# Performance work log

Hardware: AMD Instinct MI355X
Metric: run time of the kernel (lower is better)

## Reference

```python
import jax, jax.numpy as jnp
import numpy as np

EMBED_DIM = 1024
NUM_HEADS = 16
HEAD_DIM = EMBED_DIM // NUM_HEADS
D_FF = 4096
N, T, S = 4, 2048, 2048


def _linear_params(key, d_in, d_out):
    k1, k2 = jax.random.split(key)
    bound = 1.0 / np.sqrt(d_in)
    W = jax.random.uniform(k1, (d_in, d_out), minval=-bound, maxval=bound, dtype=jnp.float32)
    b = jax.random.uniform(k2, (d_out,), minval=-bound, maxval=bound, dtype=jnp.float32)
    return W, b


def setup_inputs() -> dict:
    key = jax.random.key(0)
    ks = jax.random.split(key, 20)
    inp = {
        'tgt': jax.random.normal(ks[0], (N, T, EMBED_DIM), dtype=jnp.float32),
        'memory': jax.random.normal(ks[1], (N, S, EMBED_DIM), dtype=jnp.float32),
        'tgt_mask': jnp.tril(jnp.ones((T, T), dtype=jnp.float32)),
    }
    # self-attn params
    for i, nm in enumerate(['sa_Wq', 'sa_Wk', 'sa_Wv', 'sa_A', 'ca_Wq', 'ca_Wk', 'ca_Wv', 'ca_A']):
        W, b = _linear_params(ks[2 + i], EMBED_DIM, EMBED_DIM)
        inp[nm] = W
        inp[nm + '_b'] = b
    W1, b1 = _linear_params(ks[10], EMBED_DIM, D_FF)
    W2, b2 = _linear_params(ks[11], D_FF, EMBED_DIM)
    inp.update(lin1_W=W1, lin1_b=b1, lin2_W=W2, lin2_b=b2)
    for i in (1, 2, 3):
        inp[f'ln{i}_g'] = jnp.ones((EMBED_DIM,), dtype=jnp.float32)
        inp[f'ln{i}_b'] = jnp.zeros((EMBED_DIM,), dtype=jnp.float32)
    return inp


def _layer_norm(x, g, b, eps=1e-5):
    mu = jnp.mean(x, axis=-1, keepdims=True)
    var = jnp.var(x, axis=-1, keepdims=True)
    return (x - mu) * jax.lax.rsqrt(var + eps) * g + b


def _mha(query, key, value, Wq, bq, Wk, bk, Wv, bv, Wa, ba, mask=None):
    Nq, Tq, D = query.shape
    Tk = key.shape[1]
    q = (query @ Wq + bq).reshape(Nq, Tq, NUM_HEADS, HEAD_DIM)
    k = (key @ Wk + bk).reshape(Nq, Tk, NUM_HEADS, HEAD_DIM)
    v = (value @ Wv + bv).reshape(Nq, Tk, NUM_HEADS, HEAD_DIM)
    attn = jnp.einsum('bthd,bshd->bhts', q, k) / np.sqrt(HEAD_DIM)
    if mask is not None:
        attn = jnp.where(mask == 0, -jnp.inf, attn)
    score = jax.nn.softmax(attn, axis=-1)
    y = jnp.einsum('bhts,bshd->bthd', score, v).reshape(Nq, Tq, D)
    return y @ Wa + ba


def reference(tgt, memory, tgt_mask,
              sa_Wq, sa_Wq_b, sa_Wk, sa_Wk_b, sa_Wv, sa_Wv_b, sa_A, sa_A_b,
              ca_Wq, ca_Wq_b, ca_Wk, ca_Wk_b, ca_Wv, ca_Wv_b, ca_A, ca_A_b,
              lin1_W, lin1_b, lin2_W, lin2_b,
              ln1_g, ln1_b, ln2_g, ln2_b, ln3_g, ln3_b):
    t2 = _mha(tgt, tgt, tgt, sa_Wq, sa_Wq_b, sa_Wk, sa_Wk_b, sa_Wv, sa_Wv_b, sa_A, sa_A_b, tgt_mask)
    x = _layer_norm(tgt + t2, ln1_g, ln1_b)
    t2 = _mha(x, memory, memory, ca_Wq, ca_Wq_b, ca_Wk, ca_Wk_b, ca_Wv, ca_Wv_b, ca_A, ca_A_b)
    x = _layer_norm(x + t2, ln2_g, ln2_b)
    t2 = jax.nn.relu(x @ lin1_W + lin1_b) @ lin2_W + lin2_b
    return _layer_norm(x + t2, ln3_g, ln3_b)
```

## Files before the change

kernel.cpp:

```cpp
#include <hip/hip_runtime.h>

typedef __bf16 bf16;
typedef __bf16 bf16x4 __attribute__((ext_vector_type(4)));
typedef __bf16 bf16x8 __attribute__((ext_vector_type(8)));
typedef float  f32x4  __attribute__((ext_vector_type(4)));

#define EMBED 1024
#define HEADS 16
#define HDIM  64
#define DFF   4096
#define BATCH 4
#define SEQ   2048
#define MROWS 8192

__global__ __launch_bounds__(256) void cvt_kernel(
    const float* __restrict__ x, bf16* __restrict__ y, int n)
{
  int i = (blockIdx.x * 256 + threadIdx.x) * 8;
  if (i >= n) return;
  float4 a = *(const float4*)(x + i);
  float4 b = *(const float4*)(x + i + 4);
  bf16x8 v;
  v[0] = (bf16)a.x; v[1] = (bf16)a.y; v[2] = (bf16)a.z; v[3] = (bf16)a.w;
  v[4] = (bf16)b.x; v[5] = (bf16)b.y; v[6] = (bf16)b.z; v[7] = (bf16)b.w;
  *(bf16x8*)(y + i) = v;
}

__global__ __launch_bounds__(256) void wt_kernel(
    const float* __restrict__ W, bf16* __restrict__ Wt, int K, int N)
{
  __shared__ __align__(16) float Ls[64 * 68];
  const int k0 = blockIdx.x * 64, n0 = blockIdx.y * 64;
  const int ty = threadIdx.x >> 4, tx = threadIdx.x & 15;
  #pragma unroll
  for (int r = 0; r < 4; ++r) {
    const int k = ty + r * 16;
    float4 v = *(const float4*)(W + (size_t)(k0 + k) * N + n0 + tx * 4);
    *(float4*)(Ls + k * 68 + tx * 4) = v;
  }
  __syncthreads();
  #pragma unroll
  for (int it = 0; it < 2; ++it) {
    const int c = it * 256 + threadIdx.x;
    const int n = c >> 3, kc = (c & 7) * 8;
    bf16x8 v;
    #pragma unroll
    for (int j = 0; j < 8; ++j) v[j] = (bf16)Ls[(kc + j) * 68 + n];
    *(bf16x8*)(Wt + (size_t)(n0 + n) * K + k0 + kc) = v;
  }
}

__global__ void cat3_kernel(float* __restrict__ dst, const float* __restrict__ a,
                            const float* __restrict__ b, const float* __restrict__ c, int n)
{
  int i = blockIdx.x * 256 + threadIdx.x;
  if (i < n) dst[i] = a[i];
  else if (i < 2 * n) dst[i] = b[i - n];
  else if (c && i < 3 * n) dst[i] = c[i - 2 * n];
}

__global__ __launch_bounds__(256) void vtr_kernel(
    const bf16* __restrict__ V, int ldv, bf16* __restrict__ Vt, int Skv)
{
  __shared__ __align__(16) bf16 Ls[64 * 72];
  const int k0 = blockIdx.x * 64;
  const int bh = blockIdx.y, b = bh >> 4, h = bh & 15;
  const int t = threadIdx.x;
  {
    const int key = t >> 2, dc = (t & 3) * 16;
    const bf16* src = V + (size_t)(b * Skv + k0 + key) * ldv + h * HDIM + dc;
    bf16x8 a0 = *(const bf16x8*)src;
    bf16x8 a1 = *(const bf16x8*)(src + 8);
    *(bf16x8*)(Ls + key * 72 + dc) = a0;
    *(bf16x8*)(Ls + key * 72 + dc + 8) = a1;
  }
  __syncthreads();
  {
    const int d = t >> 2, kc = (t & 3) * 16;
    bf16x8 v0, v1;
    #pragma unroll
    for (int j = 0; j < 8; ++j) v0[j] = Ls[(kc + j) * 72 + d];
    #pragma unroll
    for (int j = 0; j < 8; ++j) v1[j] = Ls[(kc + 8 + j) * 72 + d];
    bf16* dst = Vt + ((size_t)(bh * HDIM + d)) * Skv + k0 + kc;
    *(bf16x8*)dst = v0;
    *(bf16x8*)(dst + 8) = v1;
  }
}

__device__ __forceinline__ void gll16(const bf16* g, bf16* l) {
  __builtin_amdgcn_global_load_lds(
      (const __attribute__((address_space(1))) unsigned*)g,
      (__attribute__((address_space(3))) unsigned*)l, 16, 0, 0);
}

__global__ __launch_bounds__(256) void gemm128(
    const bf16* __restrict__ A, int lda, const bf16* __restrict__ Bt, int ldb,
    const float* __restrict__ bias, const bf16* __restrict__ res_b,
    const float* __restrict__ res_f, bf16* __restrict__ out_b,
    float* __restrict__ out_f, int N, int K, int relu)
{
  __shared__ __align__(16) bf16 As[128 * 32];
  __shared__ __align__(16) bf16 Bs[128 * 32];
  const int tid  = threadIdx.x;
  const int lane = tid & 63, wave = tid >> 6;
  const int quad = lane >> 4, l16 = lane & 15;
  const int wm = wave & 1, wn = wave >> 1;
  const int m0 = blockIdx.y * 128, n0 = blockIdx.x * 128;

  const int c0row = tid >> 2, c0kc = (tid & 3) * 8;
  const int c1row = (256 + tid) >> 2, c1kc = c0kc;

  f32x4 acc[4][4];
  #pragma unroll
  for (int i = 0; i < 4; ++i)
    #pragma unroll
    for (int j = 0; j < 4; ++j) acc[i][j] = f32x4{0, 0, 0, 0};

  for (int k0 = 0; k0 < K; k0 += 32) {
    gll16(A  + (size_t)(m0 + c0row) * lda + k0 + c0kc, As + (size_t)(wave * 64) * 8);
    gll16(Bt + (size_t)(n0 + c0row) * ldb + k0 + c0kc, Bs + (size_t)(wave * 64) * 8);
    gll16(A  + (size_t)(m0 + c1row) * lda + k0 + c1kc, As + (size_t)(256 + wave * 64) * 8);
    gll16(Bt + (size_t)(n0 + c1row) * ldb + k0 + c1kc, Bs + (size_t)(256 + wave * 64) * 8);
    __syncthreads();

    bf16x8 af[4], bfr[4];
    #pragma unroll
    for (int i = 0; i < 4; ++i)
      af[i] = *(const bf16x8*)(As + (wm * 64 + i * 16 + l16) * 32 + quad * 8);
    #pragma unroll
    for (int j = 0; j < 4; ++j)
      bfr[j] = *(const bf16x8*)(Bs + (wn * 64 + j * 16 + l16) * 32 + quad * 8);
    #pragma unroll
    for (int i = 0; i < 4; ++i)
      #pragma unroll
      for (int j = 0; j < 4; ++j)
        acc[i][j] = __builtin_amdgcn_mfma_f32_16x16x32_bf16(af[i], bfr[j], acc[i][j], 0, 0, 0);
    __syncthreads();
  }

  #pragma unroll
  for (int j = 0; j < 4; ++j) {
    const int col = n0 + wn * 64 + j * 16 + l16;
    const float bv = bias ? bias[col] : 0.f;
    #pragma unroll
    for (int i = 0; i < 4; ++i) {
      #pragma unroll
      for (int r = 0; r < 4; ++r) {
        const int row = m0 + wm * 64 + i * 16 + quad * 4 + r;
        const size_t idx = (size_t)row * N + col;
        float v = acc[i][j][r] + bv;
        if (res_b) v += (float)res_b[idx];
        if (res_f) v += res_f[idx];
        if (relu)  v = fmaxf(v, 0.f);
        if (out_b) out_b[idx] = (bf16)v;
        if (out_f) out_f[idx] = v;
      }
    }
  }
}

__global__ __launch_bounds__(256) void ln_kernel(
    const float* __restrict__ x, const float* __restrict__ g, const float* __restrict__ b,
    bf16* __restrict__ out_b, float* __restrict__ out_f)
{
  __shared__ float red[8];
  const int tid = threadIdx.x, lane = tid & 63, wave = tid >> 6;
  const float* xr = x + (size_t)blockIdx.x * EMBED;
  float4 v = *(const float4*)(xr + tid * 4);
  float vv[4] = {v.x, v.y, v.z, v.w};
  float s  = vv[0] + vv[1] + vv[2] + vv[3];
  float s2 = vv[0]*vv[0] + vv[1]*vv[1] + vv[2]*vv[2] + vv[3]*vv[3];
  #pragma unroll
  for (int off = 32; off >= 1; off >>= 1) {
    s  += __shfl_xor(s, off);
    s2 += __shfl_xor(s2, off);
  }
  if (lane == 0) { red[wave] = s; red[4 + wave] = s2; }
  __syncthreads();
  s  = red[0] + red[1] + red[2] + red[3];
  s2 = red[4] + red[5] + red[6] + red[7];
  const float mu  = s * (1.f / EMBED);
  const float var = s2 * (1.f / EMBED) - mu * mu;
  const float rs  = rsqrtf(fmaxf(var, 0.f) + 1e-5f);
  #pragma unroll
  for (int i = 0; i < 4; ++i) {
    const int col = tid * 4 + i;
    const float o = (vv[i] - mu) * rs * g[col] + b[col];
    const size_t idx = (size_t)blockIdx.x * EMBED + col;
    if (out_b) out_b[idx] = (bf16)o;
    if (out_f) out_f[idx] = o;
  }
}

__global__ __launch_bounds__(256) void fattn_kernel(
    const bf16* __restrict__ Q, int ldq, const bf16* __restrict__ K, int ldk,
    const bf16* __restrict__ Vt, bf16* __restrict__ Y, int Skv, int causal)
{
  constexpr int PLD = 72;
  __shared__ __align__(16) bf16 Ks[2][64 * 64];
  __shared__ __align__(16) bf16 Vs[2][64 * 64];
  __shared__ __align__(16) bf16 Ps[4 * 32 * PLD];

  const int tid  = threadIdx.x;
  const int lane = tid & 63, wave = tid >> 6;
  const int quad = lane >> 4, l16 = lane & 15;
  const int q0 = blockIdx.x * 128;
  const int bh = blockIdx.y, b = bh >> 4, h = bh & 15;
  const int wq0 = q0 + wave * 32;

  const bf16* Kb = K + (size_t)b * Skv * ldk + h * HDIM;
  const bf16* Vb = Vt + (size_t)(bh * HDIM) * Skv;

  const int sr = lane >> 3;
  const int se = ((lane & 7) ^ sr) << 3;

  const int sw  = l16 & 7;
  const int co0 = (quad ^ sw) << 3;
  const int co1 = ((4 + quad) ^ sw) << 3;

  auto stage = [&](int kt, int buf) {
    const int k0 = kt * 64;
    const int r0 = wave * 16;
    gll16(Kb + (size_t)(k0 + r0 + sr) * ldk + se,     &Ks[buf][(r0)     * 64]);
    gll16(Kb + (size_t)(k0 + r0 + 8 + sr) * ldk + se, &Ks[buf][(r0 + 8) * 64]);
    gll16(Vb + (size_t)(r0 + sr) * Skv + k0 + se,     &Vs[buf][(r0)     * 64]);
    gll16(Vb + (size_t)(r0 + 8 + sr) * Skv + k0 + se, &Vs[buf][(r0 + 8) * 64]);
  };

  bf16x8 qf[2][2];
  #pragma unroll
  for (int i = 0; i < 2; ++i) {
    const bf16* qp = Q + (size_t)(b * SEQ + wq0 + i * 16 + l16) * ldq + h * HDIM;
    qf[i][0] = *(const bf16x8*)(qp + quad * 8);
    qf[i][1] = *(const bf16x8*)(qp + 32 + quad * 8);
  }

  f32x4 O[2][4];
  float m_run[2], l_run[2];
  #pragma unroll
  for (int i = 0; i < 2; ++i)
    #pragma unroll
    for (int nt = 0; nt < 4; ++nt) O[i][nt] = f32x4{0, 0, 0, 0};
  #pragma unroll
  for (int i = 0; i < 2; ++i) { m_run[i] = -1e30f; l_run[i] = 0.f; }

  bf16* Pw = Ps + wave * 32 * PLD;
  const int nkt = causal ? (q0 / 64 + 2) : (Skv / 64);

  stage(0, 0);
  __syncthreads();

  for (int kt = 0; kt < nkt; ++kt) {
    const int cur = kt & 1;
    const int k0 = kt * 64;
    if (kt + 1 < nkt) stage(kt + 1, cur ^ 1);

    const bf16* Kc = Ks[cur];
    const bf16* Vc = Vs[cur];

    f32x4 s[2][4];
    __builtin_amdgcn_s_setprio(1);
    #pragma unroll
    for (int nt = 0; nt < 4; ++nt) {
      const int row = nt * 16 + l16;
      bf16x8 kf0 = *(const bf16x8*)(Kc + row * 64 + co0);
      bf16x8 kf1 = *(const bf16x8*)(Kc + row * 64 + co1);
      #pragma unroll
      for (int i = 0; i < 2; ++i) {
        f32x4 t = f32x4{0, 0, 0, 0};
        t = __builtin_amdgcn_mfma_f32_16x16x32_bf16(kf0, qf[i][0], t, 0, 0, 0);
        t = __builtin_amdgcn_mfma_f32_16x16x32_bf16(kf1, qf[i][1], t, 0, 0, 0);
        s[i][nt] = t;
      }
    }
    __builtin_amdgcn_s_setprio(0);

    const bool diag = causal && (k0 + 63 > wq0);
    #pragma unroll
    for (int i = 0; i < 2; ++i) {
      const int q = wq0 + i * 16 + l16;
      #pragma unroll
      for (int nt = 0; nt < 4; ++nt) {
        #pragma unroll
        for (int r = 0; r < 4; ++r) {
          float v = s[i][nt][r] * 0.125f;
          const int key = k0 + nt * 16 + quad * 4 + r;
          if (diag && key > q) v = -1e30f;
          s[i][nt][r] = v;
        }
      }
    }

    #pragma unroll
    for (int i = 0; i < 2; ++i) {
      float pm = s[i][0][0];
      #pragma unroll
      for (int nt = 0; nt < 4; ++nt)
        #pragma unroll
        for (int r = 0; r < 4; ++r) pm = fmaxf(pm, s[i][nt][r]);
      pm = fmaxf(pm, __shfl_xor(pm, 16));
      pm = fmaxf(pm, __shfl_xor(pm, 32));
      const float m_new = fmaxf(m_run[i], pm);
      const float al = __expf(m_run[i] - m_new);
      m_run[i] = m_new;
      float ls = 0.f;
      #pragma unroll
      for (int nt = 0; nt < 4; ++nt) {
        #pragma unroll
        for (int r = 0; r < 4; ++r) {
          const float e = __expf(s[i][nt][r] - m_new);
          s[i][nt][r] = e;
          ls += e;
        }
      }
      ls += __shfl_xor(ls, 16);
      ls += __shfl_xor(ls, 32);
      l_run[i] = l_run[i] * al + ls;
      #pragma unroll
      for (int nt = 0; nt < 4; ++nt) {
        bf16x4 pk;
        pk[0] = (bf16)s[i][nt][0]; pk[1] = (bf16)s[i][nt][1];
        pk[2] = (bf16)s[i][nt][2]; pk[3] = (bf16)s[i][nt][3];
        *(bf16x4*)(Pw + (i * 16 + l16) * PLD + nt * 16 + quad * 4) = pk;
      }
      float alo[4];
      #pragma unroll
      for (int r = 0; r < 4; ++r) alo[r] = __shfl(al, quad * 4 + r);
      #pragma unroll
      for (int nt = 0; nt < 4; ++nt)
        #pragma unroll
        for (int r = 0; r < 4; ++r) O[i][nt][r] *= alo[r];
    }

    bf16x8 pf[2][2];
    #pragma unroll
    for (int i = 0; i < 2; ++i) {
      pf[i][0] = *(const bf16x8*)(Pw + (i * 16 + l16) * PLD + quad * 8);
      pf[i][1] = *(const bf16x8*)(Pw + (i * 16 + l16) * PLD + 32 + quad * 8);
    }
    __builtin_amdgcn_s_setprio(1);
    #pragma unroll
    for (int nt = 0; nt < 4; ++nt) {
      const int row = nt * 16 + l16;
      bf16x8 vf0 = *(const bf16x8*)(Vc + row * 64 + co0);
      bf16x8 vf1 = *(const bf16x8*)(Vc + row * 64 + co1);
      #pragma unroll
      for (int i = 0; i < 2; ++i) {
        O[i][nt] = __builtin_amdgcn_mfma_f32_16x16x32_bf16(pf[i][0], vf0, O[i][nt], 0, 0, 0);
        O[i][nt] = __builtin_amdgcn_mfma_f32_16x16x32_bf16(pf[i][1], vf1, O[i][nt], 0, 0, 0);
      }
    }
    __builtin_amdgcn_s_setprio(0);
    __syncthreads();
  }

  #pragma unroll
  for (int i = 0; i < 2; ++i) {
    float inv[4];
    #pragma unroll
    for (int r = 0; r < 4; ++r) {
      const float lv = __shfl(l_run[i], quad * 4 + r);
      inv[r] = 1.f / lv;
    }
    #pragma unroll
    for (int nt = 0; nt < 4; ++nt) {
      #pragma unroll
      for (int r = 0; r < 4; ++r) {
        const int q = wq0 + i * 16 + quad * 4 + r;
        Y[((size_t)(b * SEQ + q)) * EMBED + h * HDIM + nt * 16 + l16] = (bf16)(O[i][nt][r] * inv[r]);
      }
    }
  }
}

__global__ void fill_kernel(float* out, float v, int n) {
  int i = blockIdx.x * 256 + threadIdx.x;
  if (i < n) out[i] = v;
}

extern "C" void kernel_launch(void* const* d_in, const int* in_sizes, int n_in,
                              void* d_out, int out_size, void* d_ws, size_t ws_size,
                              hipStream_t stream)
{
  const float* tgt    = (const float*)d_in[0];
  const float* mem    = (const float*)d_in[1];
  const float* sa_Wq  = (const float*)d_in[3];
  const float* sa_Wqb = (const float*)d_in[4];
  const float* sa_Wk  = (const float*)d_in[5];
  const float* sa_Wkb = (const float*)d_in[6];
  const float* sa_Wv  = (const float*)d_in[7];
  const float* sa_Wvb = (const float*)d_in[8];
  const float* sa_A   = (const float*)d_in[9];
  const float* sa_Ab  = (const float*)d_in[10];
  const float* ca_Wq  = (const float*)d_in[11];
  const float* ca_Wqb = (const float*)d_in[12];
  const float* ca_Wk  = (const float*)d_in[13];
  const float* ca_Wkb = (const float*)d_in[14];
  const float* ca_Wv  = (const float*)d_in[15];
  const float* ca_Wvb = (const float*)d_in[16];
  const float* ca_A   = (const float*)d_in[17];
  const float* ca_Ab  = (const float*)d_in[18];
  const float* l1W    = (const float*)d_in[19];
  const float* l1b    = (const float*)d_in[20];
  const float* l2W    = (const float*)d_in[21];
  const float* l2b    = (const float*)d_in[22];
  const float* g1     = (const float*)d_in[23];
  const float* b1     = (const float*)d_in[24];
  const float* g2     = (const float*)d_in[25];
  const float* b2     = (const float*)d_in[26];
  const float* g3     = (const float*)d_in[27];
  const float* b3     = (const float*)d_in[28];

  const size_t MB = 1024 * 1024;
  const size_t NEED = 80 * MB + 4096;
  if (ws_size < NEED) {
    fill_kernel<<<(out_size + 255) / 256, 256, 0, stream>>>((float*)d_out, 3.0f, out_size);
    return;
  }

  char* ws = (char*)d_ws;
  const size_t MD = (size_t)MROWS * EMBED;
  bf16*  qkv   = (bf16*)ws;
  bf16*  yb    = (bf16*)(ws + 48 * MB);
  bf16*  wqkvt = (bf16*)(ws + 48 * MB);
  float* qkvbias = (float*)(ws + 54 * MB + 512 * 1024);
  bf16*  kvb   = (bf16*)ws;
  bf16*  qB    = (bf16*)(ws + 32 * MB);
  bf16*  wkvt  = (bf16*)(ws + 48 * MB);
  bf16*  wqt   = (bf16*)(ws + 52 * MB);
  float* kvbias = (float*)(ws + 54 * MB + 512 * 1024);
  bf16*  awt   = (bf16*)ws;
  bf16*  xb    = (bf16*)(ws + 64 * MB);
  bf16*  hb    = (bf16*)ws;
  bf16*  l1t   = (bf16*)(ws + 32 * MB);
  bf16*  l2t   = (bf16*)(ws + 40 * MB);
  float* P   = (float*)d_out;
  bf16*  inb = (bf16*)d_out;
  bf16*  vtg = (bf16*)((char*)d_out + 16 * MB);

  dim3 blk(256);
  dim3 gQKV(3072 / 128, MROWS / 128);
  dim3 gKV(2048 / 128, MROWS / 128);
  dim3 gEE(EMBED / 128, MROWS / 128);
  dim3 gF1(2048 / 128, MROWS / 128);
  dim3 gAT(SEQ / 128, BATCH * HEADS);
  dim3 gVT(SEQ / 64, BATCH * HEADS);
  dim3 gWee(16, 16);
  const int ncv = (int)(MD / 8 / 256);

  cvt_kernel<<<ncv, blk, 0, stream>>>(tgt, inb, (int)MD);
  wt_kernel<<<gWee, blk, 0, stream>>>(sa_Wq, wqkvt, EMBED, EMBED);
  wt_kernel<<<gWee, blk, 0, stream>>>(sa_Wk, wqkvt + 1024 * 1024, EMBED, EMBED);
  wt_kernel<<<gWee, blk, 0, stream>>>(sa_Wv, wqkvt + 2 * 1024 * 1024, EMBED, EMBED);
  cat3_kernel<<<12, blk, 0, stream>>>(qkvbias, sa_Wqb, sa_Wkb, sa_Wvb, EMBED);
  gemm128<<<gQKV, blk, 0, stream>>>(inb, EMBED, wqkvt, EMBED, qkvbias, nullptr, nullptr, qkv, nullptr, 3072, EMBED, 0);
  vtr_kernel<<<gVT, blk, 0, stream>>>(qkv + 2048, 3072, vtg, SEQ);
  fattn_kernel<<<gAT, blk, 0, stream>>>(qkv, 3072, qkv + 1024, 3072, vtg, yb, SEQ, 1);
  wt_kernel<<<gWee, blk, 0, stream>>>(sa_A, awt, EMBED, EMBED);
  gemm128<<<gEE, blk, 0, stream>>>(yb, EMBED, awt, EMBED, sa_Ab, nullptr, tgt, nullptr, P, EMBED, EMBED, 0);
  ln_kernel<<<MROWS, blk, 0, stream>>>(P, g1, b1, xb, nullptr);

  cvt_kernel<<<ncv, blk, 0, stream>>>(mem, inb, (int)MD);
  wt_kernel<<<gWee, blk, 0, stream>>>(ca_Wk, wkvt, EMBED, EMBED);
  wt_kernel<<<gWee, blk, 0, stream>>>(ca_Wv, wkvt + 1024 * 1024, EMBED, EMBED);
  wt_kernel<<<gWee, blk, 0, stream>>>(ca_Wq, wqt, EMBED, EMBED);
  cat3_kernel<<<8, blk, 0, stream>>>(kvbias, ca_Wkb, ca_Wvb, nullptr, EMBED);
  gemm128<<<gKV, blk, 0, stream>>>(inb, EMBED, wkvt, EMBED, kvbias, nullptr, nullptr, kvb, nullptr, 2048, EMBED, 0);
  gemm128<<<gEE, blk, 0, stream>>>(xb, EMBED, wqt, EMBED, ca_Wqb, nullptr, nullptr, qB, nullptr, EMBED, EMBED, 0);
  vtr_kernel<<<gVT, blk, 0, stream>>>(kvb + 1024, 2048, vtg, SEQ);
  fattn_kernel<<<gAT, blk, 0, stream>>>(qB, 1024, kvb, 2048, vtg, yb, SEQ, 0);
  wt_kernel<<<gWee, blk, 0, stream>>>(ca_A, awt, EMBED, EMBED);
  gemm128<<<gEE, blk, 0, stream>>>(yb, EMBED, awt, EMBED, ca_Ab, xb, nullptr, nullptr, P, EMBED, EMBED, 0);
  ln_kernel<<<MROWS, blk, 0, stream>>>(P, g2, b2, xb, nullptr);

  wt_kernel<<<dim3(16, 64), blk, 0, stream>>>(l1W, l1t, EMBED, DFF);
  wt_kernel<<<dim3(64, 16), blk, 0, stream>>>(l2W, l2t, DFF, EMBED);
  gemm128<<<gF1, blk, 0, stream>>>(xb, EMBED, l1t, EMBED, l1b, nullptr, nullptr, hb, nullptr, 2048, EMBED, 1);
  gemm128<<<gEE, blk, 0, stream>>>(hb, 2048, l2t, DFF, l2b, xb, nullptr, nullptr, P, EMBED, 2048, 0);
  gemm128<<<gF1, blk, 0, stream>>>(xb, EMBED, l1t + (size_t)2048 * 1024, EMBED, l1b + 2048, nullptr, nullptr, hb, nullptr, 2048, EMBED, 1);
  gemm128<<<gEE, blk, 0, stream>>>(hb, 2048, l2t + 2048, DFF, nullptr, nullptr, P, nullptr, P, EMBED, 2048, 0);
  ln_kernel<<<MROWS, blk, 0, stream>>>(P, g3, b3, nullptr, (float*)d_out);
}
```

Before: 1.203 ms.

## Add 256x256 GEMM tile kernel for wide projections and fold attention scale into exp

Adds a 512-thread GEMM with 256x256 output tiles, double-buffered LDS staging, phased MFMA issue and XCD-aware workgroup remapping. It is used for the QKV, cross-attention KV and FFN-up projections, to raise arithmetic intensity and cut global/LDS traffic per FLOP. Separately, flash attention drops the per-element 0.125 scale multiply and the masked select on non-diagonal tiles, folding the scale into an fmaf inside the exponent. The large tiles use 64KB of shared memory per buffer pair and many accumulator registers, which can lower occupancy, and grids become small (e.g. 256 blocks for N=2048).

```diff
diff --git a/kernel.cpp b/kernel.cpp
--- a/kernel.cpp
+++ b/kernel.cpp
@@ -160,6 +160,125 @@
   }
 }
 
+__global__ __launch_bounds__(512, 2) void gemm256(
+    const bf16* __restrict__ A, int lda, const bf16* __restrict__ Bt, int ldb,
+    const float* __restrict__ bias, const bf16* __restrict__ res_b,
+    const float* __restrict__ res_f, bf16* __restrict__ out_b,
+    float* __restrict__ out_f, int N, int K, int relu)
+{
+  __shared__ __align__(16) bf16 As[2][256 * 64];
+  __shared__ __align__(16) bf16 Bs[2][256 * 64];
+  const int tid  = threadIdx.x;
+  const int lane = tid & 63, wave = tid >> 6;
+  const int quad = lane >> 4, l16 = lane & 15;
+  const int wm = wave & 1, wn = wave >> 1;
+
+  const int gx   = gridDim.x;
+  const int nwg  = gx * gridDim.y;
+  const int flat = blockIdx.y * gx + blockIdx.x;
+  const int qc = nwg >> 3, rc = nwg & 7;
+  const int xcd = flat & 7, off = flat >> 3;
+  const int wg = (xcd < rc ? xcd * (qc + 1) : rc * (qc + 1) + (xcd - rc) * qc) + off;
+  const int m0 = (wg / gx) * 256, n0 = (wg % gx) * 256;
+
+  const int sr8 = lane >> 3;
+  const int se  = ((lane & 7) ^ sr8) << 3;
+
+  const int sw  = l16 & 7;
+  const int co0 = (quad ^ sw) << 3;
+  const int co1 = ((4 + quad) ^ sw) << 3;
+
+  f32x4 acc[8][4];
+  #pragma unroll
+  for (int i = 0; i < 8; ++i)
+    #pragma unroll
+    for (int j = 0; j < 4; ++j) acc[i][j] = f32x4{0, 0, 0, 0};
+
+  const int ntile = K >> 6;
+
+  auto stageA = [&](int t, int buf) {
+    const int k0 = t << 6;
+    #pragma unroll
+    for (int g = 0; g < 4; ++g) {
+      const int rr = g * 64 + wave * 8;
+      gll16(A + (size_t)(m0 + rr + sr8) * lda + k0 + se, &As[buf][(size_t)rr * 64]);
+    }
+  };
+  auto stageB = [&](int t, int buf) {
+    const int k0 = t << 6;
+    #pragma unroll
+    for (int g = 0; g < 4; ++g) {
+      const int rr = g * 64 + wave * 8;
+      gll16(Bt + (size_t)(n0 + rr + sr8) * ldb + k0 + se, &Bs[buf][(size_t)rr * 64]);
+    }
+  };
+
+  stageA(0, 0);
+  stageB(0, 0);
+  __syncthreads();
+
+  for (int t = 0; t < ntile; ++t) {
+    const int cur = t & 1;
+    const bf16* Ac = As[cur];
+    const bf16* Bc = Bs[cur];
+    #pragma unroll
+    for (int ph = 0; ph < 4; ++ph) {
+      const int ih = ph >> 1, jh = ph & 1;
+      bf16x8 af[4][2], bfrag[2][2];
+      #pragma unroll
+      for (int ii = 0; ii < 4; ++ii) {
+        const int row = wm * 128 + (ih * 4 + ii) * 16 + l16;
+        af[ii][0] = *(const bf16x8*)(Ac + row * 64 + co0);
+        af[ii][1] = *(const bf16x8*)(Ac + row * 64 + co1);
+      }
+      #pragma unroll
+      for (int jj = 0; jj < 2; ++jj) {
+        const int row = wn * 64 + (jh * 2 + jj) * 16 + l16;
+        bfrag[jj][0] = *(const bf16x8*)(Bc + row * 64 + co0);
+        bfrag[jj][1] = *(const bf16x8*)(Bc + row * 64 + co1);
+      }
+      if (t + 1 < ntile) {
+        if (ph == 0) stageA(t + 1, cur ^ 1);
+        else if (ph == 1) stageB(t + 1, cur ^ 1);
+      }
+      __builtin_amdgcn_s_barrier();
+      __builtin_amdgcn_s_setprio(1);
+      #pragma unroll
+      for (int ii = 0; ii < 4; ++ii)
+        #pragma unroll
+        for (int jj = 0; jj < 2; ++jj) {
+          acc[ih * 4 + ii][jh * 2 + jj] = __builtin_amdgcn_mfma_f32_16x16x32_bf16(
+              af[ii][0], bfrag[jj][0], acc[ih * 4 + ii][jh * 2 + jj], 0, 0, 0);
+          acc[ih * 4 + ii][jh * 2 + jj] = __builtin_amdgcn_mfma_f32_16x16x32_bf16(
+              af[ii][1], bfrag[jj][1], acc[ih * 4 + ii][jh * 2 + jj], 0, 0, 0);
+        }
+      __builtin_amdgcn_s_setprio(0);
+      __builtin_amdgcn_s_barrier();
+    }
+    __syncthreads();
+  }
+
+  #pragma unroll
+  for (int j = 0; j < 4; ++j) {
+    const int col = n0 + wn * 64 + j * 16 + l16;
+    const float bv = bias ? bias[col] : 0.f;
+    #pragma unroll
+    for (int i = 0; i < 8; ++i) {
+      #pragma unroll
+      for (int r = 0; r < 4; ++r) {
+        const int row = m0 + wm * 128 + i * 16 + quad * 4 + r;
+        const size_t idx = (size_t)row * N + col;
+        float v = acc[i][j][r] + bv;
+        if (res_b) v += (float)res_b[idx];
+        if (res_f) v += res_f[idx];
+        if (relu)  v = fmaxf(v, 0.f);
+        if (out_b) out_b[idx] = (bf16)v;
+        if (out_f) out_f[idx] = v;
+      }
+    }
+  }
+}
+
 __global__ __launch_bounds__(256) void ln_kernel(
     const float* __restrict__ x, const float* __restrict__ g, const float* __restrict__ b,
     bf16* __restrict__ out_b, float* __restrict__ out_f)
@@ -276,18 +395,17 @@
     }
     __builtin_amdgcn_s_setprio(0);
 
-    const bool diag = causal && (k0 + 63 > wq0);
-    #pragma unroll
-    for (int i = 0; i < 2; ++i) {
-      const int q = wq0 + i * 16 + l16;
-      #pragma unroll
-      for (int nt = 0; nt < 4; ++nt) {
+    if (causal && (k0 + 63 > wq0)) {
+      #pragma unroll
+      for (int i = 0; i < 2; ++i) {
+        const int q = wq0 + i * 16 + l16;
         #pragma unroll
-        for (int r = 0; r < 4; ++r) {
-          float v = s[i][nt][r] * 0.125f;
-          const int key = k0 + nt * 16 + quad * 4 + r;
-          if (diag && key > q) v = -1e30f;
-          s[i][nt][r] = v;
+        for (int nt = 0; nt < 4; ++nt) {
+          #pragma unroll
+          for (int r = 0; r < 4; ++r) {
+            const int key = k0 + nt * 16 + quad * 4 + r;
+            if (key > q) s[i][nt][r] = -1e30f;
+          }
         }
       }
     }
@@ -302,14 +420,15 @@
       pm = fmaxf(pm, __shfl_xor(pm, 16));
       pm = fmaxf(pm, __shfl_xor(pm, 32));
       const float m_new = fmaxf(m_run[i], pm);
-      const float al = __expf(m_run[i] - m_new);
+      const float al = __expf((m_run[i] - m_new) * 0.125f);
       m_run[i] = m_new;
+      const float mc = m_new * 0.125f;
       float ls = 0.f;
       #pragma unroll
       for (int nt = 0; nt < 4; ++nt) {
         #pragma unroll
         for (int r = 0; r < 4; ++r) {
-          const float e = __expf(s[i][nt][r] - m_new);
+          const float e = __expf(fmaf(s[i][nt][r], 0.125f, -mc));
           s[i][nt][r] = e;
           ls += e;
         }
@@ -440,10 +559,11 @@
   bf16*  vtg = (bf16*)((char*)d_out + 16 * MB);
 
   dim3 blk(256);
-  dim3 gQKV(3072 / 128, MROWS / 128);
-  dim3 gKV(2048 / 128, MROWS / 128);
+  dim3 blk512(512);
+  dim3 gQKV(3072 / 256, MROWS / 256);
+  dim3 gKV(2048 / 256, MROWS / 256);
   dim3 gEE(EMBED / 128, MROWS / 128);
-  dim3 gF1(2048 / 128, MROWS / 128);
+  dim3 gF1(2048 / 256, MROWS / 256);
   dim3 gAT(SEQ / 128, BATCH * HEADS);
   dim3 gVT(SEQ / 64, BATCH * HEADS);
   dim3 gWee(16, 16);
@@ -454,7 +574,7 @@
   wt_kernel<<<gWee, blk, 0, stream>>>(sa_Wk, wqkvt + 1024 * 1024, EMBED, EMBED);
   wt_kernel<<<gWee, blk, 0, stream>>>(sa_Wv, wqkvt + 2 * 1024 * 1024, EMBED, EMBED);
   cat3_kernel<<<12, blk, 0, stream>>>(qkvbias, sa_Wqb, sa_Wkb, sa_Wvb, EMBED);
-  gemm128<<<gQKV, blk, 0, stream>>>(inb, EMBED, wqkvt, EMBED, qkvbias, nullptr, nullptr, qkv, nullptr, 3072, EMBED, 0);
+  gemm256<<<gQKV, blk512, 0, stream>>>(inb, EMBED, wqkvt, EMBED, qkvbias, nullptr, nullptr, qkv, nullptr, 3072, EMBED, 0);
   vtr_kernel<<<gVT, blk, 0, stream>>>(qkv + 2048, 3072, vtg, SEQ);
   fattn_kernel<<<gAT, blk, 0, stream>>>(qkv, 3072, qkv + 1024, 3072, vtg, yb, SEQ, 1);
   wt_kernel<<<gWee, blk, 0, stream>>>(sa_A, awt, EMBED, EMBED);
@@ -466,7 +586,7 @@
   wt_kernel<<<gWee, blk, 0, stream>>>(ca_Wv, wkvt + 1024 * 1024, EMBED, EMBED);
   wt_kernel<<<gWee, blk, 0, stream>>>(ca_Wq, wqt, EMBED, EMBED);
   cat3_kernel<<<8, blk, 0, stream>>>(kvbias, ca_Wkb, ca_Wvb, nullptr, EMBED);
-  gemm128<<<gKV, blk, 0, stream>>>(inb, EMBED, wkvt, EMBED, kvbias, nullptr, nullptr, kvb, nullptr, 2048, EMBED, 0);
+  gemm256<<<gKV, blk512, 0, stream>>>(inb, EMBED, wkvt, EMBED, kvbias, nullptr, nullptr, kvb, nullptr, 2048, EMBED, 0);
   gemm128<<<gEE, blk, 0, stream>>>(xb, EMBED, wqt, EMBED, ca_Wqb, nullptr, nullptr, qB, nullptr, EMBED, EMBED, 0);
   vtr_kernel<<<gVT, blk, 0, stream>>>(kvb + 1024, 2048, vtg, SEQ);
   fattn_kernel<<<gAT, blk, 0, stream>>>(qB, 1024, kvb, 2048, vtg, yb, SEQ, 0);
@@ -476,9 +596,9 @@
 
   wt_kernel<<<dim3(16, 64), blk, 0, stream>>>(l1W, l1t, EMBED, DFF);
   wt_kernel<<<dim3(64, 16), blk, 0, stream>>>(l2W, l2t, DFF, EMBED);
-  gemm128<<<gF1, blk, 0, stream>>>(xb, EMBED, l1t, EMBED, l1b, nullptr, nullptr, hb, nullptr, 2048, EMBED, 1);
+  gemm256<<<gF1, blk512, 0, stream>>>(xb, EMBED, l1t, EMBED, l1b, nullptr, nullptr, hb, nullptr, 2048, EMBED, 1);
   gemm128<<<gEE, blk, 0, stream>>>(hb, 2048, l2t, DFF, l2b, xb, nullptr, nullptr, P, EMBED, 2048, 0);
-  gemm128<<<gF1, blk, 0, stream>>>(xb, EMBED, l1t + (size_t)2048 * 1024, EMBED, l1b + 2048, nullptr, nullptr, hb, nullptr, 2048, EMBED, 1);
+  gemm256<<<gF1, blk512, 0, stream>>>(xb, EMBED, l1t + (size_t)2048 * 1024, EMBED, l1b + 2048, nullptr, nullptr, hb, nullptr, 2048, EMBED, 1);
   gemm128<<<gEE, blk, 0, stream>>>(hb, 2048, l2t + 2048, DFF, nullptr, nullptr, P, nullptr, P, EMBED, 2048, 0);
   ln_kernel<<<MROWS, blk, 0, stream>>>(P, g3, b3, nullptr, (float*)d_out);
 }
```

New measurement: 1.253 ms. 4.2% more time.

## Double-buffer GEMM LDS tiles and pair causal attention query tiles for balance

Applied to the files above, without the earlier changes.

The GEMM kernel now double-buffers its A/B LDS tiles and prefetches the next K-slice while computing the current one, removing one barrier per iteration and overlapping loads with MFMA. The causal attention kernel launches half as many blocks, each processing a short and a long query tile (x and 15-x), so every block does equal work and the grid tail is reduced. The softmax scale is folded into the exponent via fma instead of a separate multiply. It doubles GEMM LDS use, which may lower occupancy, and halves the number of causal attention blocks.

```diff
diff --git a/kernel.cpp b/kernel.cpp
--- a/kernel.cpp
+++ b/kernel.cpp
@@ -100,8 +100,8 @@
     const float* __restrict__ res_f, bf16* __restrict__ out_b,
     float* __restrict__ out_f, int N, int K, int relu)
 {
-  __shared__ __align__(16) bf16 As[128 * 32];
-  __shared__ __align__(16) bf16 Bs[128 * 32];
+  __shared__ __align__(16) bf16 As[2][128 * 32];
+  __shared__ __align__(16) bf16 Bs[2][128 * 32];
   const int tid  = threadIdx.x;
   const int lane = tid & 63, wave = tid >> 6;
   const int quad = lane >> 4, l16 = lane & 15;
@@ -109,7 +109,12 @@
   const int m0 = blockIdx.y * 128, n0 = blockIdx.x * 128;
 
   const int c0row = tid >> 2, c0kc = (tid & 3) * 8;
-  const int c1row = (256 + tid) >> 2, c1kc = c0kc;
+  const int c1row = 64 + c0row;
+
+  const bf16* a0 = A  + (size_t)(m0 + c0row) * lda + c0kc;
+  const bf16* b0 = Bt + (size_t)(n0 + c0row) * ldb + c0kc;
+  const bf16* a1 = A  + (size_t)(m0 + c1row) * lda + c0kc;
+  const bf16* b1 = Bt + (size_t)(n0 + c1row) * ldb + c0kc;
 
   f32x4 acc[4][4];
   #pragma unroll
@@ -117,20 +122,28 @@
     #pragma unroll
     for (int j = 0; j < 4; ++j) acc[i][j] = f32x4{0, 0, 0, 0};
 
-  for (int k0 = 0; k0 < K; k0 += 32) {
-    gll16(A  + (size_t)(m0 + c0row) * lda + k0 + c0kc, As + (size_t)(wave * 64) * 8);
-    gll16(Bt + (size_t)(n0 + c0row) * ldb + k0 + c0kc, Bs + (size_t)(wave * 64) * 8);
-    gll16(A  + (size_t)(m0 + c1row) * lda + k0 + c1kc, As + (size_t)(256 + wave * 64) * 8);
-    gll16(Bt + (size_t)(n0 + c1row) * ldb + k0 + c1kc, Bs + (size_t)(256 + wave * 64) * 8);
-    __syncthreads();
+  auto stage = [&](int k0, int buf) {
+    gll16(a0 + k0, As[buf] + wave * 512);
+    gll16(b0 + k0, Bs[buf] + wave * 512);
+    gll16(a1 + k0, As[buf] + 2048 + wave * 512);
+    gll16(b1 + k0, Bs[buf] + 2048 + wave * 512);
+  };
+
+  const int nk = K >> 5;
+  stage(0, 0);
+  __syncthreads();
+
+  for (int t = 0; t < nk; ++t) {
+    const int cur = t & 1;
+    if (t + 1 < nk) stage((t + 1) << 5, cur ^ 1);
 
     bf16x8 af[4], bfr[4];
     #pragma unroll
     for (int i = 0; i < 4; ++i)
-      af[i] = *(const bf16x8*)(As + (wm * 64 + i * 16 + l16) * 32 + quad * 8);
+      af[i] = *(const bf16x8*)(As[cur] + (wm * 64 + i * 16 + l16) * 32 + quad * 8);
     #pragma unroll
     for (int j = 0; j < 4; ++j)
-      bfr[j] = *(const bf16x8*)(Bs + (wn * 64 + j * 16 + l16) * 32 + quad * 8);
+      bfr[j] = *(const bf16x8*)(Bs[cur] + (wn * 64 + j * 16 + l16) * 32 + quad * 8);
     #pragma unroll
     for (int i = 0; i < 4; ++i)
       #pragma unroll
@@ -205,9 +218,7 @@
   const int tid  = threadIdx.x;
   const int lane = tid & 63, wave = tid >> 6;
   const int quad = lane >> 4, l16 = lane & 15;
-  const int q0 = blockIdx.x * 128;
   const int bh = blockIdx.y, b = bh >> 4, h = bh & 15;
-  const int wq0 = q0 + wave * 32;
 
   const bf16* Kb = K + (size_t)b * Skv * ldk + h * HDIM;
   const bf16* Vb = Vt + (size_t)(bh * HDIM) * Skv;
@@ -228,147 +239,157 @@
     gll16(Vb + (size_t)(r0 + 8 + sr) * Skv + k0 + se, &Vs[buf][(r0 + 8) * 64]);
   };
 
-  bf16x8 qf[2][2];
-  #pragma unroll
-  for (int i = 0; i < 2; ++i) {
-    const bf16* qp = Q + (size_t)(b * SEQ + wq0 + i * 16 + l16) * ldq + h * HDIM;
-    qf[i][0] = *(const bf16x8*)(qp + quad * 8);
-    qf[i][1] = *(const bf16x8*)(qp + 32 + quad * 8);
-  }
-
-  f32x4 O[2][4];
-  float m_run[2], l_run[2];
-  #pragma unroll
-  for (int i = 0; i < 2; ++i)
-    #pragma unroll
-    for (int nt = 0; nt < 4; ++nt) O[i][nt] = f32x4{0, 0, 0, 0};
-  #pragma unroll
-  for (int i = 0; i < 2; ++i) { m_run[i] = -1e30f; l_run[i] = 0.f; }
-
   bf16* Pw = Ps + wave * 32 * PLD;
-  const int nkt = causal ? (q0 / 64 + 2) : (Skv / 64);
-
-  stage(0, 0);
-  __syncthreads();
-
-  for (int kt = 0; kt < nkt; ++kt) {
-    const int cur = kt & 1;
-    const int k0 = kt * 64;
-    if (kt + 1 < nkt) stage(kt + 1, cur ^ 1);
-
-    const bf16* Kc = Ks[cur];
-    const bf16* Vc = Vs[cur];
-
-    f32x4 s[2][4];
-    __builtin_amdgcn_s_setprio(1);
-    #pragma unroll
-    for (int nt = 0; nt < 4; ++nt) {
-      const int row = nt * 16 + l16;
-      bf16x8 kf0 = *(const bf16x8*)(Kc + row * 64 + co0);
-      bf16x8 kf1 = *(const bf16x8*)(Kc + row * 64 + co1);
+  const int npass = causal ? 2 : 1;
+
+  for (int pass = 0; pass < npass; ++pass) {
+    const int qt = causal ? (pass == 0 ? (int)blockIdx.x
+                                       : (SEQ / 128 - 1 - (int)blockIdx.x))
+                          : (int)blockIdx.x;
+    const int q0  = qt * 128;
+    const int wq0 = q0 + wave * 32;
+
+    bf16x8 qf[2][2];
+    #pragma unroll
+    for (int i = 0; i < 2; ++i) {
+      const bf16* qp = Q + (size_t)(b * SEQ + wq0 + i * 16 + l16) * ldq + h * HDIM;
+      qf[i][0] = *(const bf16x8*)(qp + quad * 8);
+      qf[i][1] = *(const bf16x8*)(qp + 32 + quad * 8);
+    }
+
+    f32x4 O[2][4];
+    float m_run[2], l_run[2];
+    #pragma unroll
+    for (int i = 0; i < 2; ++i)
+      #pragma unroll
+      for (int nt = 0; nt < 4; ++nt) O[i][nt] = f32x4{0, 0, 0, 0};
+    #pragma unroll
+    for (int i = 0; i < 2; ++i) { m_run[i] = -1e30f; l_run[i] = 0.f; }
+
+    const int nkt = causal ? (q0 / 64 + 2) : (Skv / 64);
+
+    stage(0, 0);
+    __syncthreads();
+
+    for (int kt = 0; kt < nkt; ++kt) {
+      const int cur = kt & 1;
+      const int k0 = kt * 64;
+      if (kt + 1 < nkt) stage(kt + 1, cur ^ 1);
+
+      const bf16* Kc = Ks[cur];
+      const bf16* Vc = Vs[cur];
+
+      f32x4 s[2][4];
+      __builtin_amdgcn_s_setprio(1);
+      #pragma unroll
+      for (int nt = 0; nt < 4; ++nt) {
+        const int row = nt * 16 + l16;
+        bf16x8 kf0 = *(const bf16x8*)(Kc + row * 64 + co0);
+        bf16x8 kf1 = *(const bf16x8*)(Kc + row * 64 + co1);
+        #pragma unroll
+        for (int i = 0; i < 2; ++i) {
+          f32x4 t = f32x4{0, 0, 0, 0};
+          t = __builtin_amdgcn_mfma_f32_16x16x32_bf16(kf0, qf[i][0], t, 0, 0, 0);
+          t = __builtin_amdgcn_mfma_f32_16x16x32_bf16(kf1, qf[i][1], t, 0, 0, 0);
+          s[i][nt] = t;
+        }
+      }
+      __builtin_amdgcn_s_setprio(0);
+
+      if (causal && (k0 + 63 > wq0)) {
+        #pragma unroll
+        for (int i = 0; i < 2; ++i) {
+          const int q = wq0 + i * 16 + l16;
+          #pragma unroll
+          for (int nt = 0; nt < 4; ++nt) {
+            #pragma unroll
+            for (int r = 0; r < 4; ++r) {
+              const int key = k0 + nt * 16 + quad * 4 + r;
+              if (key > q) s[i][nt][r] = -1e30f;
+            }
+          }
+        }
+      }
+
       #pragma unroll
       for (int i = 0; i < 2; ++i) {
-        f32x4 t = f32x4{0, 0, 0, 0};
-        t = __builtin_amdgcn_mfma_f32_16x16x32_bf16(kf0, qf[i][0], t, 0, 0, 0);
-        t = __builtin_amdgcn_mfma_f32_16x16x32_bf16(kf1, qf[i][1], t, 0, 0, 0);
-        s[i][nt] = t;
-      }
+        float pm = s[i][0][0];
+        #pragma unroll
+        for (int nt = 0; nt < 4; ++nt)
+          #pragma unroll
+          for (int r = 0; r < 4; ++r) pm = fmaxf(pm, s[i][nt][r]);
+        pm = fmaxf(pm, __shfl_xor(pm, 16));
+        pm = fmaxf(pm, __shfl_xor(pm, 32));
+        const float m_new = fmaxf(m_run[i], pm);
+        const float al = __expf((m_run[i] - m_new) * 0.125f);
+        m_run[i] = m_new;
+        const float mc = m_new * 0.125f;
+        float ls = 0.f;
+        #pragma unroll
+        for (int nt = 0; nt < 4; ++nt) {
+          #pragma unroll
+          for (int r = 0; r < 4; ++r) {
+            const float e = __expf(fmaf(s[i][nt][r], 0.125f, -mc));
+            s[i][nt][r] = e;
+            ls += e;
+          }
+        }
+        ls += __shfl_xor(ls, 16);
+        ls += __shfl_xor(ls, 32);
+        l_run[i] = l_run[i] * al + ls;
+        #pragma unroll
+        for (int nt = 0; nt < 4; ++nt) {
+          bf16x4 pk;
+          pk[0] = (bf16)s[i][nt][0]; pk[1] = (bf16)s[i][nt][1];
+          pk[2] = (bf16)s[i][nt][2]; pk[3] = (bf16)s[i][nt][3];
+          *(bf16x4*)(Pw + (i * 16 + l16) * PLD + nt * 16 + quad * 4) = pk;
+        }
+        float alo[4];
+        #pragma unroll
+        for (int r = 0; r < 4; ++r) alo[r] = __shfl(al, quad * 4 + r);
+        #pragma unroll
+        for (int nt = 0; nt < 4; ++nt)
+          #pragma unroll
+          for (int r = 0; r < 4; ++r) O[i][nt][r] *= alo[r];
+      }
+
+      bf16x8 pf[2][2];
+      #pragma unroll
+      for (int i = 0; i < 2; ++i) {
+        pf[i][0] = *(const bf16x8*)(Pw + (i * 16 + l16) * PLD + quad * 8);
+        pf[i][1] = *(const bf16x8*)(Pw + (i * 16 + l16) * PLD + 32 + quad * 8);
+      }
+      __builtin_amdgcn_s_setprio(1);
+      #pragma unroll
+      for (int nt = 0; nt < 4; ++nt) {
+        const int row = nt * 16 + l16;
+        bf16x8 vf0 = *(const bf16x8*)(Vc + row * 64 + co0);
+        bf16x8 vf1 = *(const bf16x8*)(Vc + row * 64 + co1);
+        #pragma unroll
+        for (int i = 0; i < 2; ++i) {
+          O[i][nt] = __builtin_amdgcn_mfma_f32_16x16x32_bf16(pf[i][0], vf0, O[i][nt], 0, 0, 0);
+          O[i][nt] = __builtin_amdgcn_mfma_f32_16x16x32_bf16(pf[i][1], vf1, O[i][nt], 0, 0, 0);
+        }
+      }
+      __builtin_amdgcn_s_setprio(0);
+      __syncthreads();
     }
-    __builtin_amdgcn_s_setprio(0);
-
-    const bool diag = causal && (k0 + 63 > wq0);
+
     #pragma unroll
     for (int i = 0; i < 2; ++i) {
-      const int q = wq0 + i * 16 + l16;
+      float inv[4];
+      #pragma unroll
+      for (int r = 0; r < 4; ++r) {
+        const float lv = __shfl(l_run[i], quad * 4 + r);
+        inv[r] = 1.f / lv;
+      }
       #pragma unroll
       for (int nt = 0; nt < 4; ++nt) {
         #pragma unroll
         for (int r = 0; r < 4; ++r) {
-          float v = s[i][nt][r] * 0.125f;
-          const int key = k0 + nt * 16 + quad * 4 + r;
-          if (diag && key > q) v = -1e30f;
-          s[i][nt][r] = v;
+          const int q = wq0 + i * 16 + quad * 4 + r;
+          Y[((size_t)(b * SEQ + q)) * EMBED + h * HDIM + nt * 16 + l16] = (bf16)(O[i][nt][r] * inv[r]);
         }
-      }
-    }
-
-    #pragma unroll
-    for (int i = 0; i < 2; ++i) {
-      float pm = s[i][0][0];
-      #pragma unroll
-      for (int nt = 0; nt < 4; ++nt)
-        #pragma unroll
-        for (int r = 0; r < 4; ++r) pm = fmaxf(pm, s[i][nt][r]);
-      pm = fmaxf(pm, __shfl_xor(pm, 16));
-      pm = fmaxf(pm, __shfl_xor(pm, 32));
-      const float m_new = fmaxf(m_run[i], pm);
-      const float al = __expf(m_run[i] - m_new);
-      m_run[i] = m_new;
-      float ls = 0.f;
-      #pragma unroll
-      for (int nt = 0; nt < 4; ++nt) {
-        #pragma unroll
-        for (int r = 0; r < 4; ++r) {
-          const float e = __expf(s[i][nt][r] - m_new);
-          s[i][nt][r] = e;
-          ls += e;
-        }
-      }
-      ls += __shfl_xor(ls, 16);
-      ls += __shfl_xor(ls, 32);
-      l_run[i] = l_run[i] * al + ls;
-      #pragma unroll
-      for (int nt = 0; nt < 4; ++nt) {
-        bf16x4 pk;
-        pk[0] = (bf16)s[i][nt][0]; pk[1] = (bf16)s[i][nt][1];
-        pk[2] = (bf16)s[i][nt][2]; pk[3] = (bf16)s[i][nt][3];
-        *(bf16x4*)(Pw + (i * 16 + l16) * PLD + nt * 16 + quad * 4) = pk;
-      }
-      float alo[4];
-      #pragma unroll
-      for (int r = 0; r < 4; ++r) alo[r] = __shfl(al, quad * 4 + r);
-      #pragma unroll
-      for (int nt = 0; nt < 4; ++nt)
-        #pragma unroll
-        for (int r = 0; r < 4; ++r) O[i][nt][r] *= alo[r];
-    }
-
-    bf16x8 pf[2][2];
-    #pragma unroll
-    for (int i = 0; i < 2; ++i) {
-      pf[i][0] = *(const bf16x8*)(Pw + (i * 16 + l16) * PLD + quad * 8);
-      pf[i][1] = *(const bf16x8*)(Pw + (i * 16 + l16) * PLD + 32 + quad * 8);
-    }
-    __builtin_amdgcn_s_setprio(1);
-    #pragma unroll
-    for (int nt = 0; nt < 4; ++nt) {
-      const int row = nt * 16 + l16;
-      bf16x8 vf0 = *(const bf16x8*)(Vc + row * 64 + co0);
-      bf16x8 vf1 = *(const bf16x8*)(Vc + row * 64 + co1);
-      #pragma unroll
-      for (int i = 0; i < 2; ++i) {
-        O[i][nt] = __builtin_amdgcn_mfma_f32_16x16x32_bf16(pf[i][0], vf0, O[i][nt], 0, 0, 0);
-        O[i][nt] = __builtin_amdgcn_mfma_f32_16x16x32_bf16(pf[i][1], vf1, O[i][nt], 0, 0, 0);
-      }
-    }
-    __builtin_amdgcn_s_setprio(0);
-    __syncthreads();
-  }
-
-  #pragma unroll
-  for (int i = 0; i < 2; ++i) {
-    float inv[4];
-    #pragma unroll
-    for (int r = 0; r < 4; ++r) {
-      const float lv = __shfl(l_run[i], quad * 4 + r);
-      inv[r] = 1.f / lv;
-    }
-    #pragma unroll
-    for (int nt = 0; nt < 4; ++nt) {
-      #pragma unroll
-      for (int r = 0; r < 4; ++r) {
-        const int q = wq0 + i * 16 + quad * 4 + r;
-        Y[((size_t)(b * SEQ + q)) * EMBED + h * HDIM + nt * 16 + l16] = (bf16)(O[i][nt][r] * inv[r]);
       }
     }
   }
@@ -444,6 +465,7 @@
   dim3 gKV(2048 / 128, MROWS / 128);
   dim3 gEE(EMBED / 128, MROWS / 128);
   dim3 gF1(2048 / 128, MROWS / 128);
+  dim3 gATC(SEQ / 256, BATCH * HEADS);
   dim3 gAT(SEQ / 128, BATCH * HEADS);
   dim3 gVT(SEQ / 64, BATCH * HEADS);
   dim3 gWee(16, 16);
@@ -456,7 +478,7 @@
   cat3_kernel<<<12, blk, 0, stream>>>(qkvbias, sa_Wqb, sa_Wkb, sa_Wvb, EMBED);
   gemm128<<<gQKV, blk, 0, stream>>>(inb, EMBED, wqkvt, EMBED, qkvbias, nullptr, nullptr, qkv, nullptr, 3072, EMBED, 0);
   vtr_kernel<<<gVT, blk, 0, stream>>>(qkv + 2048, 3072, vtg, SEQ);
-  fattn_kernel<<<gAT, blk, 0, stream>>>(qkv, 3072, qkv + 1024, 3072, vtg, yb, SEQ, 1);
+  fattn_kernel<<<gATC, blk, 0, stream>>>(qkv, 3072, qkv + 1024, 3072, vtg, yb, SEQ, 1);
   wt_kernel<<<gWee, blk, 0, stream>>>(sa_A, awt, EMBED, EMBED);
   gemm128<<<gEE, blk, 0, stream>>>(yb, EMBED, awt, EMBED, sa_Ab, nullptr, tgt, nullptr, P, EMBED, EMBED, 0);
   ln_kernel<<<MROWS, blk, 0, stream>>>(P, g1, b1, xb, nullptr);
```

After: 1.092 ms. -9.3%, faster.
